# Kernel optimization log

Hardware: AMD Instinct MI355X
Metric: run time of the kernel (lower is better)

The kernel has to match this reference:

```python
import jax, jax.numpy as jnp
import numpy as np

N_QUBITS = 20
EVO_SUPPORT = (2, 5)
CHAIN_QUBIT = 0


def _apply_operator(state, op, support):
    """Apply batched operator op (2^k, 2^k, B) to state (2,)*n + (B,) on `support` qubits.

    Faithful to pyqtorch's apply_operator: reshape op to (2,)*2k + (B,) and contract
    the support axes, keeping the batch axis aligned.
    """
    n = state.ndim - 1
    k = len(support)
    B = state.shape[-1]
    op = op.reshape((2,) * (2 * k) + (B,))
    letters = 'abcdefghijklmnopqrstuvwxyz'
    s_l = list(letters[:n])          # state qubit axes
    b = letters[n]                   # batch axis
    out_l = list(letters[n + 1:n + 1 + k])
    in_l = [s_l[q] for q in support]
    op_str = ''.join(out_l) + ''.join(in_l) + b
    st_str = ''.join(s_l) + b
    res = list(s_l)
    for q, o in zip(support, out_l):
        res[q] = o
    return jnp.einsum(f"{op_str},{st_str}->{''.join(res) + b}", op, state)


def setup_inputs() -> dict:
    key = jax.random.key(0)
    ks = jax.random.split(key, 6)
    B = 16
    dim = 2 ** N_QUBITS
    return {
        'state_re': jax.random.normal(ks[0], (dim, B), jnp.float32),
        'state_im': jax.random.normal(ks[1], (dim, B), jnp.float32),
        'hmat_re': jax.random.normal(ks[2], (4, 4, B), jnp.float32),
        'hmat_im': jax.random.normal(ks[3], (4, 4, B), jnp.float32),
        'theta': jax.random.uniform(ks[4], (8, B), jnp.float32),
        'tvals': jax.random.uniform(ks[5], (B,), jnp.float32),
    }


def reference(state_re, state_im, hmat_re, hmat_im, theta, tvals):
    n = N_QUBITS
    B = state_re.shape[-1]
    state = (state_re + 1j * state_im).astype(jnp.complex64).reshape((2,) * n + (B,))

    # --- PyQComposedBlock: chain of single-qubit RX gates composed via reduce(bmm, reversed) ---
    half = 0.5 * theta                      # (N_ops, B)
    c = jnp.cos(half).astype(jnp.complex64)
    s = jnp.sin(half).astype(jnp.complex64)
    # U_k: [[c, -i s], [-i s, c]] per op, batch-first layout (N_ops, B, 2, 2)
    U = jnp.stack([jnp.stack([c, -1j * s], axis=-1),
                   jnp.stack([-1j * s, c], axis=-1)], axis=-2)
    acc = U[-1]
    for i in range(U.shape[0] - 2, -1, -1):  # reduce(bmm, reversed(ops)): U_{N-1} @ ... @ U_0
        acc = acc @ U[i]
    state = _apply_operator(state, jnp.moveaxis(acc, 0, -1), (CHAIN_QUBIT,))

    # --- PyQHamiltonianEvolution: U = exp(-i t H) on a 2-qubit support ---
    A = (hmat_re + 1j * hmat_im).astype(jnp.complex64)       # (4, 4, B)
    H = 0.5 * (A + jnp.conj(jnp.swapaxes(A, 0, 1)))          # Hermitian generator
    Hb = jnp.moveaxis(H, -1, 0)                              # (B, 4, 4)
    evals, V = jnp.linalg.eigh(Hb)                           # H Hermitian -> exact matrix exp
    phase = jnp.exp(-1j * tvals[:, None] * evals)            # (B, 4)
    Ue = jnp.einsum('bij,bj,bkj->bik', V, phase.astype(jnp.complex64), jnp.conj(V))
    state = _apply_operator(state, jnp.moveaxis(Ue, 0, -1), EVO_SUPPORT)

    # --- Observable: total magnetization sum_q Z_q (AddPyQOperation of diagonal Z ops) ---
    w = jnp.zeros((2,) * n, jnp.float32)
    z = jnp.array([1.0, -1.0], jnp.float32)
    for q in range(n):
        w = w + z.reshape((1,) * q + (2,) + (1,) * (n - 1 - q))
    opsi = state * w[..., None]
    # expectation Re<psi|O|psi> per batch element
    return jnp.real(jnp.sum(jnp.conj(state) * opsi, axis=tuple(range(n))))
```

## Files before the change

### kernel.cpp

```cpp
#include <hip/hip_runtime.h>
#include <math.h>

constexpr int NQ     = 20;
constexpr int DIM    = 1 << NQ;
constexpr int B      = 16;
constexpr int GROUPS = 1 << 17;
constexpr int NBLK   = 1024;
constexpr int NTHR   = 256;


__global__ void prep_kernel(const float* __restrict__ hre, const float* __restrict__ him,
                            const float* __restrict__ theta, const float* __restrict__ tv,
                            float* __restrict__ ws) {
  int b = threadIdx.x;
  if (b >= B) return;

  double th = 0.0;
  for (int k = 0; k < 8; k++) th += (double)theta[k * B + b];
  th *= 0.5;
  ws[b]     = (float)cos(th);
  ws[B + b] = (float)sin(th);

  double t = (double)tv[b];
  double Mre[4][4], Mim[4][4];
  for (int i = 0; i < 4; i++)
    for (int j = 0; j < 4; j++) {
      double are = hre[(i*4+j)*B + b], aim = him[(i*4+j)*B + b];
      double cre = hre[(j*4+i)*B + b], cim = him[(j*4+i)*B + b];
      double Hre = 0.5*(are + cre), Him = 0.5*(aim - cim);
      Mre[i][j] = t * Him;
      Mim[i][j] = -t * Hre;
    }

  double ninf = 0.0;
  for (int i = 0; i < 4; i++) {
    double r = 0.0;
    for (int j = 0; j < 4; j++) r += fabs(Mre[i][j]) + fabs(Mim[i][j]);
    ninf = fmax(ninf, r);
  }
  int sc = 0;
  while (ninf > 0.25 && sc < 40) { ninf *= 0.5; sc++; }
  double scale = ldexp(1.0, -sc);
  for (int i = 0; i < 4; i++)
    for (int j = 0; j < 4; j++) { Mre[i][j] *= scale; Mim[i][j] *= scale; }

  double Tre[4][4], Tim[4][4];
  for (int i = 0; i < 4; i++)
    for (int j = 0; j < 4; j++) { Tre[i][j] = (i==j) ? 1.0 : 0.0; Tim[i][j] = 0.0; }
  for (int k = 13; k >= 1; k--) {
    double Pre[4][4], Pim[4][4];
    double inv = 1.0 / (double)k;
    for (int i = 0; i < 4; i++)
      for (int j = 0; j < 4; j++) {
        double rr = 0.0, ii = 0.0;
        for (int m = 0; m < 4; m++) {
          rr += Mre[i][m]*Tre[m][j] - Mim[i][m]*Tim[m][j];
          ii += Mre[i][m]*Tim[m][j] + Mim[i][m]*Tre[m][j];
        }
        Pre[i][j] = rr*inv + ((i==j) ? 1.0 : 0.0);
        Pim[i][j] = ii*inv;
      }
    for (int i = 0; i < 4; i++)
      for (int j = 0; j < 4; j++) { Tre[i][j] = Pre[i][j]; Tim[i][j] = Pim[i][j]; }
  }
  for (int q = 0; q < sc; q++) {
    double Pre[4][4], Pim[4][4];
    for (int i = 0; i < 4; i++)
      for (int j = 0; j < 4; j++) {
        double rr = 0.0, ii = 0.0;
        for (int m = 0; m < 4; m++) {
          rr += Tre[i][m]*Tre[m][j] - Tim[i][m]*Tim[m][j];
          ii += Tre[i][m]*Tim[m][j] + Tim[i][m]*Tre[m][j];
        }
        Pre[i][j] = rr; Pim[i][j] = ii;
      }
    for (int i = 0; i < 4; i++)
      for (int j = 0; j < 4; j++) { Tre[i][j] = Pre[i][j]; Tim[i][j] = Pim[i][j]; }
  }

  float* ue = ws + 2*B + b*32;
  for (int i = 0; i < 4; i++)
    for (int j = 0; j < 4; j++) {
      ue[(i*4+j)*2]     = (float)Tre[i][j];
      ue[(i*4+j)*2 + 1] = (float)Tim[i][j];
    }
}

__global__ __launch_bounds__(NTHR) void fused_kernel(
    const float* __restrict__ sre, const float* __restrict__ sim,
    const float* __restrict__ ws, float* __restrict__ partial) {
  int tid = blockIdx.x * NTHR + threadIdx.x;
  int b = tid & 15;

  float c = ws[b], s = ws[B + b];
  float ur[4][4], ui[4][4];
  {
    const float* ue = ws + 2*B + b*32;
    #pragma unroll
    for (int i = 0; i < 4; i++)
      #pragma unroll
      for (int j = 0; j < 4; j++) { ur[i][j] = ue[(i*4+j)*2]; ui[i][j] = ue[(i*4+j)*2+1]; }
  }

  float acc = 0.f;
  const int total = NBLK * NTHR;
  for (int u = tid; u < GROUPS * 16; u += total) {
    int g = u >> 4;
    int base = (g & 0x3FFF) | ((g & 0xC000) << 1) | ((g & 0x10000) << 2);
    int a0 = base * B + b;

    float ar[8], ai[8];
    #pragma unroll
    for (int j = 0; j < 8; j++) {
      int off = a0 + (((((j>>2)&1) << 19) | (((j>>1)&1) << 17) | ((j&1) << 14))) * B;
      ar[j] = sre[off];
      ai[j] = sim[off];
    }

    #pragma unroll
    for (int j = 0; j < 4; j++) {
      float xr = ar[j], xi = ai[j], yr = ar[j+4], yi = ai[j+4];
      ar[j]   = c*xr + s*yi;   ai[j]   = c*xi - s*yr;
      ar[j+4] = s*xi + c*yr;   ai[j+4] = c*yi - s*xr;
    }

    int pc = __popc(base);
    float wb = (float)(17 - 2*pc);
    #pragma unroll
    for (int h = 0; h < 2; h++) {
      float w0 = wb + (h ? -1.f : 1.f);
      #pragma unroll
      for (int k = 0; k < 4; k++) {
        float rr = 0.f, ii = 0.f;
        #pragma unroll
        for (int m = 0; m < 4; m++) {
          float xr = ar[h*4+m], xi = ai[h*4+m];
          rr = fmaf(ur[k][m], xr, rr); rr = fmaf(-ui[k][m], xi, rr);
          ii = fmaf(ur[k][m], xi, ii); ii = fmaf(ui[k][m], xr, ii);
        }
        int sb = ((k>>1)&1) + (k&1);
        float w = w0 + (float)(2 - 2*sb);
        acc = fmaf(rr*rr + ii*ii, w, acc);
      }
    }
  }

  acc += __shfl_xor(acc, 16, 64);
  acc += __shfl_xor(acc, 32, 64);

  __shared__ float red[16];
  if (threadIdx.x < 16) red[threadIdx.x] = 0.f;
  __syncthreads();
  if ((threadIdx.x & 63) < 16) atomicAdd(&red[threadIdx.x & 15], acc);
  __syncthreads();
  if (threadIdx.x < 16) partial[blockIdx.x * 16 + threadIdx.x] = red[threadIdx.x];
}

__global__ void reduce_kernel(const float* __restrict__ partial, float* __restrict__ out) {
  int t = threadIdx.x;
  int b = t & 15;
  float acc = 0.f;
  for (int i = t >> 4; i < NBLK; i += 16)
    acc += partial[i * 16 + b];
  acc += __shfl_xor(acc, 16, 64);
  acc += __shfl_xor(acc, 32, 64);
  __shared__ float red[16];
  if (t < 16) red[t] = 0.f;
  __syncthreads();
  if ((t & 63) < 16) atomicAdd(&red[t & 15], acc);
  __syncthreads();
  if (t < 16) out[t] = red[t];
}

extern "C" void kernel_launch(void* const* d_in, const int* in_sizes, int n_in,
                              void* d_out, int out_size, void* d_ws, size_t ws_size,
                              hipStream_t stream) {
  const float* sre = (const float*)d_in[0];
  const float* sim = (const float*)d_in[1];
  const float* hre = (const float*)d_in[2];
  const float* him = (const float*)d_in[3];
  const float* th  = (const float*)d_in[4];
  const float* tv  = (const float*)d_in[5];

  float* ws = (float*)d_ws;
  float* partial = ws + 544;

  prep_kernel<<<1, 64, 0, stream>>>(hre, him, th, tv, ws);
  fused_kernel<<<NBLK, NTHR, 0, stream>>>(sre, sim, ws, partial);
  reduce_kernel<<<1, 256, 0, stream>>>(partial, (float*)d_out);
}
```

Measured before the change: 197.3 us.

## Vectorize state loads to float4 over four batch lanes with LDS-staged operators

Each thread now handles one group and four consecutive batch elements, loading the state with float4 reads instead of scalar strided loads. The grid-stride loop is gone: with 512 threads per block, 1024 blocks cover all groups in one pass. The evolution matrix and the cos/sin values are staged in shared memory and read as float4, which cuts per-thread register use for the operator. Register pressure from 64 loaded floats plus the unrolled math may limit occupancy, and the launch size is now tied exactly to the problem size.

```diff
diff --git a/kernel.cpp b/kernel.cpp
--- a/kernel.cpp
+++ b/kernel.cpp
@@ -6,7 +6,7 @@
 constexpr int B      = 16;
 constexpr int GROUPS = 1 << 17;
 constexpr int NBLK   = 1024;
-constexpr int NTHR   = 256;
+constexpr int NTHR   = 512;
 
 
 __global__ void prep_kernel(const float* __restrict__ hre, const float* __restrict__ him,
@@ -86,74 +86,109 @@
     }
 }
 
+#define RXPAIR(j, f) { \
+  float xr = R[j].f, xi = I[j].f, yr = R[(j)+4].f, yi = I[(j)+4].f; \
+  R[j].f     = fmaf(c4.f, xr,  s4.f * yi); \
+  I[j].f     = fmaf(c4.f, xi, -s4.f * yr); \
+  R[(j)+4].f = fmaf(s4.f, xi,  c4.f * yr); \
+  I[(j)+4].f = fmaf(c4.f, yi, -s4.f * xr); \
+}
+
+#define UE_BI(f, bi, accv) \
+  float accv = 0.f; \
+  { \
+    const float* ub = &u_lds[(b0 + (bi)) * 36]; \
+    _Pragma("unroll") \
+    for (int k = 0; k < 4; k++) { \
+      float4 u0 = *(const float4*)(ub + 8*k);        \
+      float4 u1 = *(const float4*)(ub + 8*k + 4);    \
+      float rr0 = fmaf(u0.x, R[0].f, -u0.y * I[0].f); \
+      rr0 = fmaf(u0.z, R[1].f, rr0); rr0 = fmaf(-u0.w, I[1].f, rr0); \
+      rr0 = fmaf(u1.x, R[2].f, rr0); rr0 = fmaf(-u1.y, I[2].f, rr0); \
+      rr0 = fmaf(u1.z, R[3].f, rr0); rr0 = fmaf(-u1.w, I[3].f, rr0); \
+      float ii0 = fmaf(u0.x, I[0].f, u0.y * R[0].f); \
+      ii0 = fmaf(u0.z, I[1].f, ii0); ii0 = fmaf(u0.w, R[1].f, ii0); \
+      ii0 = fmaf(u1.x, I[2].f, ii0); ii0 = fmaf(u1.y, R[2].f, ii0); \
+      ii0 = fmaf(u1.z, I[3].f, ii0); ii0 = fmaf(u1.w, R[3].f, ii0); \
+      float rr1 = fmaf(u0.x, R[4].f, -u0.y * I[4].f); \
+      rr1 = fmaf(u0.z, R[5].f, rr1); rr1 = fmaf(-u0.w, I[5].f, rr1); \
+      rr1 = fmaf(u1.x, R[6].f, rr1); rr1 = fmaf(-u1.y, I[6].f, rr1); \
+      rr1 = fmaf(u1.z, R[7].f, rr1); rr1 = fmaf(-u1.w, I[7].f, rr1); \
+      float ii1 = fmaf(u0.x, I[4].f, u0.y * R[4].f); \
+      ii1 = fmaf(u0.z, I[5].f, ii1); ii1 = fmaf(u0.w, R[5].f, ii1); \
+      ii1 = fmaf(u1.x, I[6].f, ii1); ii1 = fmaf(u1.y, R[6].f, ii1); \
+      ii1 = fmaf(u1.z, I[7].f, ii1); ii1 = fmaf(u1.w, R[7].f, ii1); \
+      int sb = (k & 1) + (k >> 1); \
+      float w0 = wb + (float)(3 - 2*sb);             \
+      accv = fmaf(fmaf(rr0, rr0, ii0*ii0), w0,       accv); \
+      accv = fmaf(fmaf(rr1, rr1, ii1*ii1), w0 - 2.f, accv); \
+    } \
+  }
+
 __global__ __launch_bounds__(NTHR) void fused_kernel(
     const float* __restrict__ sre, const float* __restrict__ sim,
     const float* __restrict__ ws, float* __restrict__ partial) {
-  int tid = blockIdx.x * NTHR + threadIdx.x;
-  int b = tid & 15;
-
-  float c = ws[b], s = ws[B + b];
-  float ur[4][4], ui[4][4];
+  __shared__ float u_lds[16 * 36];
+  __shared__ float cs_lds[32];
+  __shared__ float red[16];
+
+  int t = threadIdx.x;
   {
-    const float* ue = ws + 2*B + b*32;
-    #pragma unroll
-    for (int i = 0; i < 4; i++)
-      #pragma unroll
-      for (int j = 0; j < 4; j++) { ur[i][j] = ue[(i*4+j)*2]; ui[i][j] = ue[(i*4+j)*2+1]; }
-  }
-
-  float acc = 0.f;
-  const int total = NBLK * NTHR;
-  for (int u = tid; u < GROUPS * 16; u += total) {
-    int g = u >> 4;
-    int base = (g & 0x3FFF) | ((g & 0xC000) << 1) | ((g & 0x10000) << 2);
-    int a0 = base * B + b;
-
-    float ar[8], ai[8];
-    #pragma unroll
-    for (int j = 0; j < 8; j++) {
-      int off = a0 + (((((j>>2)&1) << 19) | (((j>>1)&1) << 17) | ((j&1) << 14))) * B;
-      ar[j] = sre[off];
-      ai[j] = sim[off];
-    }
-
-    #pragma unroll
-    for (int j = 0; j < 4; j++) {
-      float xr = ar[j], xi = ai[j], yr = ar[j+4], yi = ai[j+4];
-      ar[j]   = c*xr + s*yi;   ai[j]   = c*xi - s*yr;
-      ar[j+4] = s*xi + c*yr;   ai[j+4] = c*yi - s*xr;
-    }
-
-    int pc = __popc(base);
-    float wb = (float)(17 - 2*pc);
-    #pragma unroll
-    for (int h = 0; h < 2; h++) {
-      float w0 = wb + (h ? -1.f : 1.f);
-      #pragma unroll
-      for (int k = 0; k < 4; k++) {
-        float rr = 0.f, ii = 0.f;
-        #pragma unroll
-        for (int m = 0; m < 4; m++) {
-          float xr = ar[h*4+m], xi = ai[h*4+m];
-          rr = fmaf(ur[k][m], xr, rr); rr = fmaf(-ui[k][m], xi, rr);
-          ii = fmaf(ur[k][m], xi, ii); ii = fmaf(ui[k][m], xr, ii);
-        }
-        int sb = ((k>>1)&1) + (k&1);
-        float w = w0 + (float)(2 - 2*sb);
-        acc = fmaf(rr*rr + ii*ii, w, acc);
-      }
-    }
-  }
-
-  acc += __shfl_xor(acc, 16, 64);
-  acc += __shfl_xor(acc, 32, 64);
-
-  __shared__ float red[16];
-  if (threadIdx.x < 16) red[threadIdx.x] = 0.f;
-  __syncthreads();
-  if ((threadIdx.x & 63) < 16) atomicAdd(&red[threadIdx.x & 15], acc);
-  __syncthreads();
-  if (threadIdx.x < 16) partial[blockIdx.x * 16 + threadIdx.x] = red[threadIdx.x];
+    int b = t >> 5, e = t & 31;
+    u_lds[b * 36 + e] = ws[2 * B + b * 32 + e];
+  }
+  if (t < 32) cs_lds[t] = ws[t];
+  if (t < 16) red[t] = 0.f;
+  __syncthreads();
+
+  int tid = blockIdx.x * NTHR + t;
+  int g   = tid >> 2;
+  int b0  = (tid & 3) << 2;
+  int base = (g & 0x3FFF) | ((g & 0xC000) << 1) | ((g & 0x10000) << 2);
+  const float* pr = sre + base * B + b0;
+  const float* pi = sim + base * B + b0;
+
+  float4 R[8], I[8];
+  #pragma unroll
+  for (int j = 0; j < 8; j++) {
+    int off = (((((j >> 2) & 1) << 19) | (((j >> 1) & 1) << 17) | ((j & 1) << 14))) * B;
+    R[j] = *(const float4*)(pr + off);
+    I[j] = *(const float4*)(pi + off);
+  }
+
+  float4 c4 = *(const float4*)&cs_lds[b0];
+  float4 s4 = *(const float4*)&cs_lds[16 + b0];
+
+  #pragma unroll
+  for (int j = 0; j < 4; j++) {
+    RXPAIR(j, x) RXPAIR(j, y) RXPAIR(j, z) RXPAIR(j, w)
+  }
+
+  int pc = __popc(base);
+  float wb = (float)(17 - 2 * pc);
+
+  UE_BI(x, 0, acc0)
+  UE_BI(y, 1, acc1)
+  UE_BI(z, 2, acc2)
+  UE_BI(w, 3, acc3)
+
+  #pragma unroll
+  for (int m = 4; m <= 32; m <<= 1) {
+    acc0 += __shfl_xor(acc0, m, 64);
+    acc1 += __shfl_xor(acc1, m, 64);
+    acc2 += __shfl_xor(acc2, m, 64);
+    acc3 += __shfl_xor(acc3, m, 64);
+  }
+
+  if ((t & 63) < 4) {
+    int bb = (t & 3) << 2;
+    atomicAdd(&red[bb + 0], acc0);
+    atomicAdd(&red[bb + 1], acc1);
+    atomicAdd(&red[bb + 2], acc2);
+    atomicAdd(&red[bb + 3], acc3);
+  }
+  __syncthreads();
+  if (t < 16) partial[blockIdx.x * 16 + t] = red[t];
 }
 
 __global__ void reduce_kernel(const float* __restrict__ partial, float* __restrict__ out) {
```

Result: faster. 191.1 us (-3.1%).
